# Kernel optimization log

Measured on AMD Instinct MI355X. Metric: run time of the kernel, lower is better.

The kernel has to match this reference:

```python
import jax, jax.numpy as jnp
import numpy as np

B, S, D, H, HD = 2, 2048, 2048, 16, 128

def _freqs_cis(dim, end, theta=10000.0):
    freqs = 1.0 / theta ** (np.arange(0, dim, 2, dtype=np.float32)[: dim // 2] / dim)
    t = np.arange(end, dtype=np.float32)
    f = np.outer(t, freqs).astype(np.float32)
    f = np.concatenate((f, f), axis=-1)
    return jnp.asarray(np.cos(f)), jnp.asarray(np.sin(f))

def _rotate_half(x):
    x1, x2 = x[..., : x.shape[-1] // 2], x[..., x.shape[-1] // 2 :]
    return jnp.concatenate((-x2, x1), axis=-1)

def setup_inputs() -> dict:
    key = jax.random.key(0)
    ks = jax.random.split(key, 5)
    x = jax.random.normal(ks[0], (B, S, D), jnp.float32)
    scale = 1.0 / np.sqrt(D)
    Wq = jax.random.normal(ks[1], (D, H, HD), jnp.float32) * scale
    Wk = jax.random.normal(ks[2], (D, H, HD), jnp.float32) * scale
    Wv = jax.random.normal(ks[3], (D, H, HD), jnp.float32) * scale
    Wo = jax.random.normal(ks[4], (H, HD, D), jnp.float32) * (1.0 / np.sqrt(D))
    mask = jnp.tril(jnp.ones((S, S), jnp.bool_))[None, None]  # causal [1,1,S,S]
    return {"x": x, "mask": mask, "Wq": Wq, "Wk": Wk, "Wv": Wv, "Wo": Wo}

def reference(x, mask, Wq, Wk, Wv, Wo):
    # QKV projections: [B,S,D] -> [B,S,H,HD]
    q = jnp.einsum('bsd,dhk->bshk', x, Wq)
    k = jnp.einsum('bsd,dhk->bshk', x, Wk)
    v = jnp.einsum('bsd,dhk->bshk', x, Wv)
    # RoPE
    cos, sin = _freqs_cis(HD, x.shape[1])
    cos = cos[None, :, None, :]
    sin = sin[None, :, None, :]
    q = q * cos + _rotate_half(q) * sin
    k = k * cos + _rotate_half(k) * sin
    # scaled dot-product attention
    scores = jnp.einsum('bqhk,bshk->bhqs', q, k) / jnp.sqrt(jnp.asarray(HD, q.dtype))
    big_neg = jnp.finfo(scores.dtype).min
    scores = jnp.where(mask, scores, big_neg)
    attn = jax.nn.softmax(scores, axis=-1)
    ctx = jnp.einsum('bhqs,bshk->bqhk', attn, v)
    # output projection contracting (heads, head_dim)
    return jnp.einsum('bqhk,hkd->bqd', ctx, Wo)
```

## Files before the change

kernel.cpp:

```cpp
#include <hip/hip_runtime.h>

typedef unsigned short u16;
typedef unsigned int u32;

constexpr int Bc = 2, Sc = 2048, Dc = 2048, Hc = 16, HDc = 128;

using short8 = __attribute__((ext_vector_type(8))) short;
using f32x4v = __attribute__((ext_vector_type(4))) float;

static __device__ __forceinline__ float bf2f(u16 v) { return __uint_as_float(((u32)v) << 16); }
static __device__ __forceinline__ u16 f2bf(float f) {
    u32 u = __float_as_uint(f);
    return (u16)((u + 0x7fffu + ((u >> 16) & 1u)) >> 16);
}

__device__ __forceinline__ void gll16(const u16* g, u16* l) {
    __builtin_amdgcn_global_load_lds((const __attribute__((address_space(1))) void*)g,
                                     (__attribute__((address_space(3))) void*)l, 16, 0, 0);
}

#define FENCE asm volatile("" ::: "memory")

__global__ __launch_bounds__(256) void rope_tab_k(float* __restrict__ ctab, float* __restrict__ stab) {
    int idx = blockIdx.x * 256 + threadIdx.x;
    int s = idx >> 6, i = idx & 63;
    float freq = exp2f(-(float)i * 0.20762050593045952f);
    float ang = (float)s * freq;
    float c, sn;
    sincosf(ang, &sn, &c);
    ctab[idx] = c;
    stab[idx] = sn;
}

__global__ __launch_bounds__(256) void cvt_k(const float* __restrict__ in, u16* __restrict__ out, int n) {
    int i = (blockIdx.x * 256 + threadIdx.x) * 8;
    if (i >= n) return;
    float4 a = *(const float4*)(in + i);
    float4 b = *(const float4*)(in + i + 4);
    u16 r[8] = {f2bf(a.x), f2bf(a.y), f2bf(a.z), f2bf(a.w),
                f2bf(b.x), f2bf(b.y), f2bf(b.z), f2bf(b.w)};
    *(uint4*)(out + i) = *(uint4*)r;
}

__global__ __launch_bounds__(256) void tcvt3_k(const float* __restrict__ in0, const float* __restrict__ in1,
                                               const float* __restrict__ in2, u16* __restrict__ out,
                                               int R, int C) {
    __shared__ u16 tile[64][68];
    const float* in = (blockIdx.z == 0) ? in0 : (blockIdx.z == 1) ? in1 : in2;
    u16* o = out + (size_t)blockIdx.z * R * C;
    int bx = blockIdx.x * 64, by = blockIdx.y * 64;
    int t = threadIdx.x;
    int r = t >> 4, c4 = (t & 15) * 4;
    #pragma unroll
    for (int i = 0; i < 4; ++i) {
        int row = by + r + i * 16;
        float4 v = *(const float4*)(in + (size_t)row * C + bx + c4);
        u16* d = &tile[r + i * 16][c4];
        d[0] = f2bf(v.x); d[1] = f2bf(v.y); d[2] = f2bf(v.z); d[3] = f2bf(v.w);
    }
    __syncthreads();
    int oc = t >> 4, r4 = (t & 15) * 4;
    #pragma unroll
    for (int i = 0; i < 4; ++i) {
        int orow = oc + i * 16;
        u16 v[4] = {tile[r4][orow], tile[r4 + 1][orow], tile[r4 + 2][orow], tile[r4 + 3][orow]};
        *(uint2*)&o[(size_t)(bx + orow) * R + by + r4] = *(const uint2*)v;
    }
}

__global__ __launch_bounds__(512, 4) void gemm_qkv32(
        const u16* __restrict__ A, const u16* __restrict__ Bt,
        u16* __restrict__ Oq, u16* __restrict__ Ok, u16* __restrict__ Ov,
        const float* __restrict__ ctab, const float* __restrict__ stab) {
    __shared__ u16 SM[33024];
    constexpr int K = Dc;
    int t = threadIdx.x, wid = t >> 6, lane = t & 63;
    int wm = wid >> 2, wn = wid & 3;
    int ln = lane & 15, lq = lane >> 4;

    int nx = gridDim.x;
    int lin = blockIdx.y * nx + blockIdx.x;
    int cpx = (nx * gridDim.y) >> 3;
    int swzb = (lin & 7) * cpx + (lin >> 3);
    int n0 = (swzb % nx) << 8;
    int m0 = (swzb / nx) << 7;

    auto stageAB = [&](int kt, int b) {
        u16* Ad = SM + b * 12288;
        u16* Bd = SM + b * 12288 + 4096;
        {
            int ci = t;
            gll16(A + (size_t)(m0 + (ci >> 2)) * K + kt * 32 + (((ci & 3) ^ ((ci >> 3) & 3)) << 3),
                  Ad + (wid * 64) * 8);
        }
        #pragma unroll
        for (int L = 0; L < 2; ++L) {
            int ci = L * 512 + t;
            gll16(Bt + (size_t)(n0 + (ci >> 2)) * K + kt * 32 + (((ci & 3) ^ ((ci >> 3) & 3)) << 3),
                  Bd + (L * 512 + wid * 64) * 8);
        }
    };

    int co = ((lq ^ ((ln >> 1) & 3)) << 3);
    f32x4v acc[4][4] = {};

    auto body = [&](const u16* Ab, const u16* Bb) {
        short8 aF[4], bF[4];
        #pragma unroll
        for (int m = 0; m < 4; ++m)
            aF[m] = *(const short8*)(Ab + (wm * 64 + m * 16 + ln) * 32 + co);
        #pragma unroll
        for (int n = 0; n < 4; ++n)
            bF[n] = *(const short8*)(Bb + (wn * 64 + n * 16 + ln) * 32 + co);
        __builtin_amdgcn_s_setprio(1);
        #pragma unroll
        for (int m = 0; m < 4; ++m)
            #pragma unroll
            for (int n = 0; n < 4; ++n)
                acc[m][n] = __builtin_amdgcn_mfma_f32_16x16x32_bf16(aF[m], bF[n], acc[m][n], 0, 0, 0);
        __builtin_amdgcn_s_setprio(0);
    };

    stageAB(0, 0);
    __syncthreads();

    #pragma unroll 1
    for (int kt = 0; kt < 64; kt += 2) {
        stageAB(kt + 1, 1);
        body(SM, SM + 4096);
        __syncthreads();
        if (kt + 2 < 64) stageAB(kt + 2, 0);
        body(SM + 12288, SM + 16384);
        __syncthreads();
    }

    int which = n0 >> 11;
    int h0 = (n0 & 2047) >> 7;
    int b_ = m0 >> 11;
    int s0 = m0 & (Sc - 1);
    u16* Es = SM;
    const int ESTR = 258;

    #pragma unroll
    for (int mf = 0; mf < 4; ++mf)
        #pragma unroll
        for (int nf = 0; nf < 4; ++nf)
            #pragma unroll
            for (int r = 0; r < 4; ++r)
                Es[(wm * 64 + mf * 16 + (lq << 2) + r) * ESTR + wn * 64 + nf * 16 + ln] =
                    f2bf(acc[mf][nf][r]);
    __syncthreads();

    if (which < 2) {
        u16* dst0 = which ? Ok : Oq;
        int u = t >> 1, h2 = t & 1;
        int r = u & 127, hh = u >> 7;
        int s = s0 + r;
        const u16* rowp = Es + r * ESTR + hh * 128;
        const float* ct = ctab + (size_t)s * 64;
        const float* st = stab + (size_t)s * 64;
        u16* dp = dst0 + (((size_t)(b_ * Hc + h0 + hh)) * Sc + s) * HDc + h2 * 64;
        #pragma unroll
        for (int j8 = 0; j8 < 64; j8 += 8) {
            uint4 aa = *(const uint4*)(rowp + j8);
            uint4 bb = *(const uint4*)(rowp + 64 + j8);
            const u16* ap8 = (const u16*)&aa;
            const u16* bp8 = (const u16*)&bb;
            float4 c0f = *(const float4*)(ct + j8);
            float4 c1f = *(const float4*)(ct + j8 + 4);
            float4 sn0 = *(const float4*)(st + j8);
            float4 sn1 = *(const float4*)(st + j8 + 4);
            float cc[8] = {c0f.x, c0f.y, c0f.z, c0f.w, c1f.x, c1f.y, c1f.z, c1f.w};
            float ss[8] = {sn0.x, sn0.y, sn0.z, sn0.w, sn1.x, sn1.y, sn1.z, sn1.w};
            u16 ov[8];
            #pragma unroll
            for (int e = 0; e < 8; ++e) {
                float x1 = bf2f(ap8[e]), x2 = bf2f(bp8[e]);
                ov[e] = h2 ? f2bf(x2 * cc[e] + x1 * ss[e]) : f2bf(x1 * cc[e] - x2 * ss[e]);
            }
            *(uint4*)(dp + j8) = *(const uint4*)ov;
        }
    } else {
        int u = t >> 1, sh = t & 1;
        int d = u & 127, hh = u >> 7;
        u16* dp = Ov + (((size_t)(b_ * Hc + h0 + hh)) * HDc + d) * Sc + s0 + sh * 64;
        #pragma unroll
        for (int r8 = 0; r8 < 64; r8 += 8) {
            u16 ov[8];
            #pragma unroll
            for (int e = 0; e < 8; ++e)
                ov[e] = Es[(sh * 64 + r8 + e) * ESTR + hh * 128 + d];
            *(uint4*)(dp + r8) = *(const uint4*)ov;
        }
    }
}


#define RDA8(P) do { _Pragma("unroll") for (int m_ = 0; m_ < 4; ++m_) { \
    aF[m_][0] = *(const short8*)((P) + m_ * 1024 + co0); \
    aF[m_][1] = *(const short8*)((P) + m_ * 1024 + co1); } } while (0)

#define RDB2(P, nh) do { _Pragma("unroll") for (int j_ = 0; j_ < 2; ++j_) { \
    bF[j_][0] = *(const short8*)((P) + ((nh) * 2 + j_) * 1024 + co0); \
    bF[j_][1] = *(const short8*)((P) + ((nh) * 2 + j_) * 1024 + co1); } } while (0)

#define MFQ8(nh) do { _Pragma("unroll") for (int m_ = 0; m_ < 4; ++m_) \
    _Pragma("unroll") for (int j_ = 0; j_ < 2; ++j_) { \
    f32x4v& c_ = acc[m_][(nh) * 2 + j_]; \
    c_ = __builtin_amdgcn_mfma_f32_16x16x32_bf16(aF[m_][0], bF[j_][0], c_, 0, 0, 0); \
    c_ = __builtin_amdgcn_mfma_f32_16x16x32_bf16(aF[m_][1], bF[j_][1], c_, 0, 0, 0); } } while (0)

#define PT(nh) do { FENCE; __builtin_amdgcn_s_barrier(); FENCE; \
    asm volatile("s_waitcnt lgkmcnt(0)" ::: "memory"); \
    __builtin_amdgcn_s_setprio(1); MFQ8(nh); __builtin_amdgcn_s_setprio(0); \
    FENCE; __builtin_amdgcn_s_barrier(); FENCE; } while (0)

#define KTILE(aRb, bRb, KST, ADST, BDST, VW) do { \
    RDA8(aRb); RDB2(bRb, 0); \
    if ((KST) >= 0) stageA(KST, ADST); \
    PT(0); \
    RDB2(bRb, 1); \
    if ((KST) >= 0) stageB(KST, BDST); \
    if ((VW) == 6) asm volatile("s_waitcnt vmcnt(6)" ::: "memory"); \
    else if ((VW) == 0) asm volatile("s_waitcnt vmcnt(0)" ::: "memory"); \
    PT(1); } while (0)

__global__ __launch_bounds__(512, 2) void gemm128_op(
        const u16* __restrict__ A, const u16* __restrict__ Bt, float* __restrict__ C2) {
    __shared__ u16 SM[73728];
    constexpr int K = Dc;
    constexpr int NT = 32;
    constexpr int N = Dc;
    int t = threadIdx.x, wid = t >> 6, lane = t & 63;
    int wm = wid >> 2, wn = wid & 3;
    int ln = lane & 15, lq = lane >> 4;

    int nx = gridDim.x;
    int lin = blockIdx.y * nx + blockIdx.x;
    int cpx = (nx * gridDim.y) >> 3;
    int swzb = (lin & 7) * cpx + (lin >> 3);
    int n0 = (swzb % nx) << 8;
    int m0 = (swzb / nx) << 7;

    u16* As0 = SM;
    u16* As1 = SM + 8192;
    u16* As2 = SM + 16384;
    u16* Bs0 = SM + 24576;
    u16* Bs1 = SM + 40960;
    u16* Bs2 = SM + 57344;

    auto stageA = [&](int kt, u16* dst) {
        #pragma unroll
        for (int L = 0; L < 2; ++L) {
            int ch16 = L * 512 + wid * 64 + lane;
            int row = ch16 >> 3, ch = ch16 & 7;
            gll16(A + (size_t)(m0 + row) * K + kt * 64 + ((ch ^ (row & 7)) << 3),
                  dst + (L * 512 + wid * 64) * 8);
        }
    };
    auto stageB = [&](int kt, u16* dst) {
        #pragma unroll
        for (int L = 0; L < 4; ++L) {
            int ch16 = L * 512 + wid * 64 + lane;
            int row = ch16 >> 3, ch = ch16 & 7;
            gll16(Bt + (size_t)(n0 + row) * K + kt * 64 + ((ch ^ (row & 7)) << 3),
                  dst + (L * 512 + wid * 64) * 8);
        }
    };

    const u16* aR0 = As0 + (wm * 64 + ln) * 64;
    const u16* aR1 = As1 + (wm * 64 + ln) * 64;
    const u16* aR2 = As2 + (wm * 64 + ln) * 64;
    const u16* bR0 = Bs0 + (wn * 64 + ln) * 64;
    const u16* bR1 = Bs1 + (wn * 64 + ln) * 64;
    const u16* bR2 = Bs2 + (wn * 64 + ln) * 64;
    int sw = ln & 7;
    int co0 = (lq ^ sw) << 3;
    int co1 = ((4 | lq) ^ sw) << 3;

    short8 aF[4][2], bF[2][2];
    f32x4v acc[4][4] = {};

    stageA(0, As0); stageB(0, Bs0);
    stageA(1, As1); stageB(1, Bs1);
    asm volatile("s_waitcnt vmcnt(6)" ::: "memory");
    FENCE; __builtin_amdgcn_s_barrier(); FENCE;

    for (int k3 = 0; k3 < NT - 2; k3 += 3) {
        KTILE(aR0, bR0, k3 + 2, As2, Bs2, 6);
        KTILE(aR1, bR1, k3 + 3, As0, Bs0, 6);
        KTILE(aR2, bR2, k3 + 4, As1, Bs1, 6);
    }
    KTILE(aR0, bR0, -1, As0, Bs0, 0);
    KTILE(aR1, bR1, -1, As0, Bs0, -1);

    int rb = m0 + wm * 64 + (lq << 2);
    int cb = n0 + wn * 64 + ln;
    #pragma unroll
    for (int mf = 0; mf < 4; ++mf)
        #pragma unroll
        for (int nf = 0; nf < 4; ++nf)
            #pragma unroll
            for (int r = 0; r < 4; ++r)
                C2[(size_t)(rb + mf * 16 + r) * N + cb + nf * 16] = acc[mf][nf][r];
}

__global__ __launch_bounds__(256) void fattn_k(const u16* __restrict__ Q, const u16* __restrict__ K,
                                               const u16* __restrict__ Vt, u16* __restrict__ ctx) {
    __shared__ u16 KsA[8192];
    __shared__ u16 VsA[8192];
    __shared__ u16 PsA[4 * 32 * 72];
    int t = threadIdx.x, wid = t >> 6, lane = t & 63;
    int bh = blockIdx.x;
    int yt = blockIdx.y;
    int qi = (yt < 8) ? yt : 23 - yt;
    int q0 = qi << 7;
    int wrow0 = q0 + wid * 32;
    const u16* Qb = Q + ((size_t)bh * Sc + wrow0) * HDc;
    const u16* Kb = K + (size_t)bh * Sc * HDc;
    const u16* Vb = Vt + (size_t)bh * HDc * Sc;
    int ln = lane & 15, lq = lane >> 4;
    u16* psw = PsA + wid * 32 * 72;

    short8 aq[2][4];
    #pragma unroll
    for (int mf = 0; mf < 2; ++mf)
        #pragma unroll
        for (int ks = 0; ks < 4; ++ks)
            aq[mf][ks] = *(const short8*)(Qb + (size_t)(mf * 16 + ln) * HDc + ks * 32 + lq * 8);

    short8 onesb;
    {
        short v = (ln == 0) ? (short)0x3F80 : (short)0;
        #pragma unroll
        for (int e = 0; e < 8; ++e) onesb[e] = v;
    }

    f32x4v o[2][8] = {};
    f32x4v lacc[2] = {};

    const float sc = 0.08838834764831845f;
    const float SHIFT = 12.0f;
    int jendw = wrow0 + 31;
    int jendb = q0 + 127;
    int swz = (ln >> 1) & 3;

    for (int j0 = 0; j0 <= jendb; j0 += 64) {
        #pragma unroll
        for (int i = 0; i < 4; ++i) {
            int p = (wid * 4 + i) * 64 + lane;
            int plane = p >> 8, key = (p >> 2) & 63;
            int qc = (p & 3) ^ ((key >> 1) & 3);
            gll16(Kb + (size_t)(j0 + key) * HDc + plane * 32 + qc * 8,
                  KsA + (size_t)(wid * 4 + i) * 512);
        }
        #pragma unroll
        for (int i = 0; i < 4; ++i) {
            int p = (wid * 4 + i) * 64 + lane;
            int plane = p >> 9, d = (p >> 2) & 127;
            int qc = (p & 3) ^ ((d >> 1) & 3);
            gll16(Vb + (size_t)d * Sc + j0 + plane * 32 + qc * 8,
                  VsA + (size_t)(wid * 4 + i) * 512);
        }
        __syncthreads();

        if (j0 <= jendw) {
            f32x4v sf[2][4] = {};
            #pragma unroll
            for (int ks = 0; ks < 4; ++ks)
                #pragma unroll
                for (int nf = 0; nf < 4; ++nf) {
                    short8 bk = *(const short8*)(KsA + ks * 2048 + (nf * 16 + ln) * 32 + ((lq ^ swz) << 3));
                    sf[0][nf] = __builtin_amdgcn_mfma_f32_16x16x32_bf16(aq[0][ks], bk, sf[0][nf], 0, 0, 0);
                    sf[1][nf] = __builtin_amdgcn_mfma_f32_16x16x32_bf16(aq[1][ks], bk, sf[1][nf], 0, 0, 0);
                }

            bool diag = (j0 + 63 > wrow0);
            #pragma unroll
            for (int mf = 0; mf < 2; ++mf) {
                int rowb = mf * 16 + (lq << 2);
                #pragma unroll
                for (int nf = 0; nf < 4; ++nf) {
                    int col = nf * 16 + ln;
                    int ck = col >> 3, cl = col & 7;
                    #pragma unroll
                    for (int r = 0; r < 4; ++r) {
                        float p = __expf(fmaf(sf[mf][nf][r], sc, -SHIFT));
                        if (diag && (j0 + col > wrow0 + rowb + r)) p = 0.f;
                        int row = rowb + r;
                        psw[row * 72 + ((ck ^ (row & 7)) << 3) + cl] = f2bf(p);
                    }
                }
            }

            short8 ap0[2][2];
            #pragma unroll
            for (int mf = 0; mf < 2; ++mf)
                #pragma unroll
                for (int ks = 0; ks < 2; ++ks)
                    ap0[mf][ks] = *(const short8*)(psw + (mf * 16 + ln) * 72 + (((ks * 4 + lq) ^ (ln & 7)) << 3));
            #pragma unroll
            for (int ks = 0; ks < 2; ++ks) {
                lacc[0] = __builtin_amdgcn_mfma_f32_16x16x32_bf16(ap0[0][ks], onesb, lacc[0], 0, 0, 0);
                lacc[1] = __builtin_amdgcn_mfma_f32_16x16x32_bf16(ap0[1][ks], onesb, lacc[1], 0, 0, 0);
                #pragma unroll
                for (int nd = 0; nd < 8; ++nd) {
                    short8 bv = *(const short8*)(VsA + ks * 4096 + (nd * 16 + ln) * 32 + ((lq ^ swz) << 3));
                    o[0][nd] = __builtin_amdgcn_mfma_f32_16x16x32_bf16(ap0[0][ks], bv, o[0][nd], 0, 0, 0);
                    o[1][nd] = __builtin_amdgcn_mfma_f32_16x16x32_bf16(ap0[1][ks], bv, o[1][nd], 0, 0, 0);
                }
            }
        }
        __syncthreads();
    }

    int b = bh >> 4, h = bh & 15;
    #pragma unroll
    for (int mf = 0; mf < 2; ++mf)
        #pragma unroll
        for (int r = 0; r < 4; ++r) {
            float lv = __shfl(lacc[mf][r], lane & 48, 64);
            float inv = 1.0f / lv;
            int q = wrow0 + mf * 16 + (lq << 2) + r;
            u16* cp = ctx + (((size_t)(b * Sc + q)) * Hc + h) * HDc + ln;
            #pragma unroll
            for (int nd = 0; nd < 8; ++nd)
                cp[nd * 16] = f2bf(o[mf][nd][r] * inv);
        }
}

extern "C" void kernel_launch(void* const* d_in, const int* in_sizes, int n_in,
                              void* d_out, int out_size, void* d_ws, size_t ws_size,
                              hipStream_t stream) {
    (void)in_sizes; (void)n_in; (void)out_size; (void)ws_size;
    const float* x  = (const float*)d_in[0];
    const float* Wq = (const float*)d_in[2];
    const float* Wk = (const float*)d_in[3];
    const float* Wv = (const float*)d_in[4];
    const float* Wo = (const float*)d_in[5];

    char* w = (char*)d_ws;
    u16* Wt  = (u16*)w; w += (size_t)3 * Dc * Dc * 2;
    u16* Qb  = (u16*)w; w += (size_t)Bc * Hc * Sc * HDc * 2;
    u16* Kb  = (u16*)w; w += (size_t)Bc * Hc * Sc * HDc * 2;
    u16* Vb  = (u16*)w; w += (size_t)Bc * Hc * Sc * HDc * 2;
    u16* ctx = (u16*)w; w += (size_t)Bc * Sc * Hc * HDc * 2;
    float* ctab = (float*)w; w += (size_t)Sc * 64 * 4;
    float* stab = (float*)w; w += (size_t)Sc * 64 * 4;
    u16* xb = (u16*)d_out;

    rope_tab_k<<<dim3(Sc * 64 / 256), 256, 0, stream>>>(ctab, stab);

    int nx = Bc * Sc * Dc;
    cvt_k<<<dim3(nx / 2048), 256, 0, stream>>>(x, xb, nx);

    tcvt3_k<<<dim3(Dc / 64, Dc / 64, 3), 256, 0, stream>>>(Wq, Wk, Wv, Wt, Dc, Dc);
    gemm_qkv32<<<dim3(3 * Dc / 256, (Bc * Sc) / 128), 512, 0, stream>>>(
        xb, Wt, Qb, Kb, Vb, ctab, stab);

    fattn_k<<<dim3(Bc * Hc, Sc / 128), 256, 0, stream>>>(Qb, Kb, Vb, ctx);

    tcvt3_k<<<dim3(Dc / 64, Dc / 64, 1), 256, 0, stream>>>(Wo, Wo, Wo, Wt, Dc, Dc);
    gemm128_op<<<dim3(Dc / 256, (Bc * Sc) / 128), 512, 0, stream>>>(
        ctx, Wt, (float*)d_out);
}
```

Baseline: 406.1 us.

## Retile QKV GEMM to 128x384 tiles with triple-buffered async LDS pipeline

The QKV projection GEMM now uses 128x384 output tiles (512 blocks, about two per CU on 256 CUs) instead of 128x256 tiles. It also replaces the double-buffered loop with a three-stage LDS pipeline that uses explicit vmcnt waits and raw barriers. The epilogue is reworked to write one 128-column head at a time through a smaller LDS staging buffer, keeping the RoPE and V-transpose outputs. The aim is fewer waves with better per-wave reuse and memory latency hidden behind MFMA, at the cost of more registers and LDS per block, lower occupancy, and a serialized three-pass epilogue.

```diff
diff --git a/kernel.cpp b/kernel.cpp
--- a/kernel.cpp
+++ b/kernel.cpp
@@ -68,130 +68,142 @@
     }
 }
 
-__global__ __launch_bounds__(512, 4) void gemm_qkv32(
+
+#define QT(RB, KST, SB, VW) do { \
+    short8 aF[4], bF[6]; \
+    _Pragma("unroll") for (int m_ = 0; m_ < 4; ++m_) \
+        aF[m_] = *(const short8*)((RB) + (wm * 64 + m_ * 16 + ln) * 32 + co); \
+    _Pragma("unroll") for (int n_ = 0; n_ < 6; ++n_) \
+        bF[n_] = *(const short8*)((RB) + 4096 + (wn * 96 + n_ * 16 + ln) * 32 + co); \
+    if ((KST) >= 0) stage((KST), (SB)); \
+    if ((VW) == 4) asm volatile("s_waitcnt vmcnt(4)" ::: "memory"); \
+    else if ((VW) == 0) asm volatile("s_waitcnt vmcnt(0)" ::: "memory"); \
+    FENCE; __builtin_amdgcn_s_barrier(); FENCE; \
+    asm volatile("s_waitcnt lgkmcnt(0)" ::: "memory"); \
+    __builtin_amdgcn_s_setprio(1); \
+    _Pragma("unroll") for (int m_ = 0; m_ < 4; ++m_) \
+    _Pragma("unroll") for (int n_ = 0; n_ < 6; ++n_) \
+        acc[m_][n_] = __builtin_amdgcn_mfma_f32_16x16x32_bf16(aF[m_], bF[n_], acc[m_][n_], 0, 0, 0); \
+    __builtin_amdgcn_s_setprio(0); \
+    FENCE; __builtin_amdgcn_s_barrier(); FENCE; \
+} while (0)
+
+__global__ __launch_bounds__(512, 2) void gemm_qkv384(
         const u16* __restrict__ A, const u16* __restrict__ Bt,
         u16* __restrict__ Oq, u16* __restrict__ Ok, u16* __restrict__ Ov,
         const float* __restrict__ ctab, const float* __restrict__ stab) {
-    __shared__ u16 SM[33024];
+    __shared__ u16 SM[49152];
     constexpr int K = Dc;
     int t = threadIdx.x, wid = t >> 6, lane = t & 63;
     int wm = wid >> 2, wn = wid & 3;
     int ln = lane & 15, lq = lane >> 4;
 
-    int nx = gridDim.x;
-    int lin = blockIdx.y * nx + blockIdx.x;
-    int cpx = (nx * gridDim.y) >> 3;
-    int swzb = (lin & 7) * cpx + (lin >> 3);
-    int n0 = (swzb % nx) << 8;
-    int m0 = (swzb / nx) << 7;
-
-    auto stageAB = [&](int kt, int b) {
-        u16* Ad = SM + b * 12288;
-        u16* Bd = SM + b * 12288 + 4096;
+    int lin = blockIdx.x;
+    int swzb = (lin & 7) * 64 + (lin >> 3);
+    int n0 = (swzb >> 5) * 384;
+    int m0 = (swzb & 31) * 128;
+
+    auto stage = [&](int kt, int b) {
+        u16* Ad = SM + b * 16384;
+        u16* Bd = SM + b * 16384 + 4096;
         {
-            int ci = t;
-            gll16(A + (size_t)(m0 + (ci >> 2)) * K + kt * 32 + (((ci & 3) ^ ((ci >> 3) & 3)) << 3),
+            int row = t >> 2, cs = t & 3;
+            gll16(A + (size_t)(m0 + row) * K + kt * 32 + ((cs ^ ((row >> 1) & 3)) << 3),
                   Ad + (wid * 64) * 8);
         }
         #pragma unroll
-        for (int L = 0; L < 2; ++L) {
+        for (int L = 0; L < 3; ++L) {
             int ci = L * 512 + t;
-            gll16(Bt + (size_t)(n0 + (ci >> 2)) * K + kt * 32 + (((ci & 3) ^ ((ci >> 3) & 3)) << 3),
+            int row = ci >> 2, cs = ci & 3;
+            gll16(Bt + (size_t)(n0 + row) * K + kt * 32 + ((cs ^ ((row >> 1) & 3)) << 3),
                   Bd + (L * 512 + wid * 64) * 8);
         }
     };
 
     int co = ((lq ^ ((ln >> 1) & 3)) << 3);
-    f32x4v acc[4][4] = {};
-
-    auto body = [&](const u16* Ab, const u16* Bb) {
-        short8 aF[4], bF[4];
-        #pragma unroll
-        for (int m = 0; m < 4; ++m)
-            aF[m] = *(const short8*)(Ab + (wm * 64 + m * 16 + ln) * 32 + co);
-        #pragma unroll
-        for (int n = 0; n < 4; ++n)
-            bF[n] = *(const short8*)(Bb + (wn * 64 + n * 16 + ln) * 32 + co);
-        __builtin_amdgcn_s_setprio(1);
-        #pragma unroll
-        for (int m = 0; m < 4; ++m)
-            #pragma unroll
-            for (int n = 0; n < 4; ++n)
-                acc[m][n] = __builtin_amdgcn_mfma_f32_16x16x32_bf16(aF[m], bF[n], acc[m][n], 0, 0, 0);
-        __builtin_amdgcn_s_setprio(0);
-    };
-
-    stageAB(0, 0);
-    __syncthreads();
+    f32x4v acc[4][6] = {};
+
+    stage(0, 0);
+    stage(1, 1);
+    asm volatile("s_waitcnt vmcnt(4)" ::: "memory");
+    FENCE; __builtin_amdgcn_s_barrier(); FENCE;
 
     #pragma unroll 1
-    for (int kt = 0; kt < 64; kt += 2) {
-        stageAB(kt + 1, 1);
-        body(SM, SM + 4096);
-        __syncthreads();
-        if (kt + 2 < 64) stageAB(kt + 2, 0);
-        body(SM + 12288, SM + 16384);
-        __syncthreads();
-    }
-
-    int which = n0 >> 11;
-    int h0 = (n0 & 2047) >> 7;
+    for (int k3 = 0; k3 < 60; k3 += 3) {
+        QT(SM,          k3 + 2, 2, 4);
+        QT(SM + 16384,  k3 + 3, 0, 4);
+        QT(SM + 32768,  k3 + 4, 1, 4);
+    }
+    QT(SM,          62, 2, 4);
+    QT(SM + 16384,  63, 0, 4);
+    QT(SM + 32768,  -1, 0, 0);
+    QT(SM,          -1, 0, -1);
+
     int b_ = m0 >> 11;
     int s0 = m0 & (Sc - 1);
     u16* Es = SM;
-    const int ESTR = 258;
-
-    #pragma unroll
-    for (int mf = 0; mf < 4; ++mf)
-        #pragma unroll
-        for (int nf = 0; nf < 4; ++nf)
-            #pragma unroll
-            for (int r = 0; r < 4; ++r)
-                Es[(wm * 64 + mf * 16 + (lq << 2) + r) * ESTR + wn * 64 + nf * 16 + ln] =
-                    f2bf(acc[mf][nf][r]);
-    __syncthreads();
-
-    if (which < 2) {
-        u16* dst0 = which ? Ok : Oq;
-        int u = t >> 1, h2 = t & 1;
-        int r = u & 127, hh = u >> 7;
-        int s = s0 + r;
-        const u16* rowp = Es + r * ESTR + hh * 128;
-        const float* ct = ctab + (size_t)s * 64;
-        const float* st = stab + (size_t)s * 64;
-        u16* dp = dst0 + (((size_t)(b_ * Hc + h0 + hh)) * Sc + s) * HDc + h2 * 64;
-        #pragma unroll
-        for (int j8 = 0; j8 < 64; j8 += 8) {
-            uint4 aa = *(const uint4*)(rowp + j8);
-            uint4 bb = *(const uint4*)(rowp + 64 + j8);
-            const u16* ap8 = (const u16*)&aa;
-            const u16* bp8 = (const u16*)&bb;
-            float4 c0f = *(const float4*)(ct + j8);
-            float4 c1f = *(const float4*)(ct + j8 + 4);
-            float4 sn0 = *(const float4*)(st + j8);
-            float4 sn1 = *(const float4*)(st + j8 + 4);
-            float cc[8] = {c0f.x, c0f.y, c0f.z, c0f.w, c1f.x, c1f.y, c1f.z, c1f.w};
-            float ss[8] = {sn0.x, sn0.y, sn0.z, sn0.w, sn1.x, sn1.y, sn1.z, sn1.w};
-            u16 ov[8];
-            #pragma unroll
-            for (int e = 0; e < 8; ++e) {
-                float x1 = bf2f(ap8[e]), x2 = bf2f(bp8[e]);
-                ov[e] = h2 ? f2bf(x2 * cc[e] + x1 * ss[e]) : f2bf(x1 * cc[e] - x2 * ss[e]);
+    const int ESTR = 130;
+
+    for (int c = 0; c < 3; ++c) {
+        #pragma unroll
+        for (int nf = 0; nf < 6; ++nf) {
+            int cg = wn * 96 + nf * 16;
+            if ((cg >> 7) == c) {
+                int col = cg & 127;
+                #pragma unroll
+                for (int mf = 0; mf < 4; ++mf)
+                    #pragma unroll
+                    for (int r = 0; r < 4; ++r)
+                        Es[(wm * 64 + mf * 16 + (lq << 2) + r) * ESTR + col + ln] =
+                            f2bf(acc[mf][nf][r]);
             }
-            *(uint4*)(dp + j8) = *(const uint4*)ov;
-        }
-    } else {
-        int u = t >> 1, sh = t & 1;
-        int d = u & 127, hh = u >> 7;
-        u16* dp = Ov + (((size_t)(b_ * Hc + h0 + hh)) * HDc + d) * Sc + s0 + sh * 64;
-        #pragma unroll
-        for (int r8 = 0; r8 < 64; r8 += 8) {
-            u16 ov[8];
-            #pragma unroll
-            for (int e = 0; e < 8; ++e)
-                ov[e] = Es[(sh * 64 + r8 + e) * ESTR + hh * 128 + d];
-            *(uint4*)(dp + r8) = *(const uint4*)ov;
-        }
+        }
+        __syncthreads();
+
+        int gcol = n0 + c * 128;
+        int which = gcol >> 11;
+        int h = (gcol & 2047) >> 7;
+        if (which < 2) {
+            u16* dst0 = which ? Ok : Oq;
+            int rh = t >> 2, h2 = t & 1, jh = (t >> 1) & 1;
+            int s = s0 + rh;
+            const u16* rowp = Es + rh * ESTR;
+            const float* ct = ctab + (size_t)s * 64;
+            const float* st = stab + (size_t)s * 64;
+            u16* dp = dst0 + (((size_t)(b_ * Hc + h)) * Sc + s) * HDc + h2 * 64;
+            #pragma unroll
+            for (int j8 = jh * 32; j8 < jh * 32 + 32; j8 += 8) {
+                uint4 aa = *(const uint4*)(rowp + j8);
+                uint4 bb = *(const uint4*)(rowp + 64 + j8);
+                const u16* ap8 = (const u16*)&aa;
+                const u16* bp8 = (const u16*)&bb;
+                float4 c0f = *(const float4*)(ct + j8);
+                float4 c1f = *(const float4*)(ct + j8 + 4);
+                float4 sn0 = *(const float4*)(st + j8);
+                float4 sn1 = *(const float4*)(st + j8 + 4);
+                float cc[8] = {c0f.x, c0f.y, c0f.z, c0f.w, c1f.x, c1f.y, c1f.z, c1f.w};
+                float ss[8] = {sn0.x, sn0.y, sn0.z, sn0.w, sn1.x, sn1.y, sn1.z, sn1.w};
+                u16 ov[8];
+                #pragma unroll
+                for (int e = 0; e < 8; ++e) {
+                    float x1 = bf2f(ap8[e]), x2 = bf2f(bp8[e]);
+                    ov[e] = h2 ? f2bf(x2 * cc[e] + x1 * ss[e]) : f2bf(x1 * cc[e] - x2 * ss[e]);
+                }
+                *(uint4*)(dp + j8) = *(const uint4*)ov;
+            }
+        } else {
+            int d = t >> 2, sh = t & 3;
+            u16* dp = Ov + (((size_t)(b_ * Hc + h)) * HDc + d) * Sc + s0 + sh * 32;
+            #pragma unroll
+            for (int r8 = 0; r8 < 32; r8 += 8) {
+                u16 ov[8];
+                #pragma unroll
+                for (int e = 0; e < 8; ++e)
+                    ov[e] = Es[(sh * 32 + r8 + e) * ESTR + d];
+                *(uint4*)(dp + r8) = *(const uint4*)ov;
+            }
+        }
+        __syncthreads();
     }
 }
 
@@ -455,8 +467,7 @@
     cvt_k<<<dim3(nx / 2048), 256, 0, stream>>>(x, xb, nx);
 
     tcvt3_k<<<dim3(Dc / 64, Dc / 64, 3), 256, 0, stream>>>(Wq, Wk, Wv, Wt, Dc, Dc);
-    gemm_qkv32<<<dim3(3 * Dc / 256, (Bc * Sc) / 128), 512, 0, stream>>>(
-        xb, Wt, Qb, Kb, Vb, ctab, stab);
+    gemm_qkv384<<<dim3(512), 512, 0, stream>>>(xb, Wt, Qb, Kb, Vb, ctab, stab);
 
     fattn_k<<<dim3(Bc * Hc, Sc / 128), 256, 0, stream>>>(Qb, Kb, Vb, ctx);
 
```

After: 393.6 us. 3.1% less time.
